# Kernel tuning notes

Hardware: AMD Instinct MI355X
Metric: run time of the kernel (lower is better)

## Reference

```python
import jax, jax.numpy as jnp
import numpy as np

N_PATCHES = 14
N_BLOCKS = 12
HIDDEN = 768
N_HEADS = 12
D_HEAD = HIDDEN // N_HEADS
MLP_RATIO = 4
OUT_D = 1000
BATCH = 32
C, H, W = 3, 224, 224
PS = H // N_PATCHES            # 16
INPUT_D = C * PS * PS          # 768
SEQ = N_PATCHES ** 2 + 1       # 197
LN_EPS = 1e-5


def _pos_emb(length, d):
    i = np.arange(length, dtype=np.float64)[:, None]
    j = np.arange(d, dtype=np.float64)[None, :]
    angle = i / (10000.0 ** ((j - (j % 2)) / d))
    pe = np.where(j % 2 == 0, np.sin(angle), np.cos(angle))
    return jnp.asarray(pe, dtype=jnp.float32)  # [length, d]


def setup_inputs() -> dict:
    key = jax.random.key(0)
    ks = jax.random.split(key, 16)
    s = 0.02
    inp = {
        "x": jax.random.normal(ks[0], (BATCH, C, H, W), jnp.float32),
        "W_map": jax.random.normal(ks[1], (INPUT_D, HIDDEN), jnp.float32) * s,
        "b_map": jnp.zeros((HIDDEN,), jnp.float32),
        "cls_tok": jax.random.uniform(ks[2], (1, HIDDEN), jnp.float32),
        "pos_emb": _pos_emb(SEQ, HIDDEN),
        "ln1_s": jnp.ones((N_BLOCKS, HIDDEN), jnp.float32),
        "ln1_b": jnp.zeros((N_BLOCKS, HIDDEN), jnp.float32),
        "Wq": jax.random.normal(ks[3], (N_BLOCKS, N_HEADS, D_HEAD, D_HEAD), jnp.float32) * s,
        "bq": jnp.zeros((N_BLOCKS, N_HEADS, D_HEAD), jnp.float32),
        "Wk": jax.random.normal(ks[4], (N_BLOCKS, N_HEADS, D_HEAD, D_HEAD), jnp.float32) * s,
        "bk": jnp.zeros((N_BLOCKS, N_HEADS, D_HEAD), jnp.float32),
        "Wv": jax.random.normal(ks[5], (N_BLOCKS, N_HEADS, D_HEAD, D_HEAD), jnp.float32) * s,
        "bv": jnp.zeros((N_BLOCKS, N_HEADS, D_HEAD), jnp.float32),
        "ln2_s": jnp.ones((N_BLOCKS, HIDDEN), jnp.float32),
        "ln2_b": jnp.zeros((N_BLOCKS, HIDDEN), jnp.float32),
        "W1": jax.random.normal(ks[6], (N_BLOCKS, HIDDEN, MLP_RATIO * HIDDEN), jnp.float32) * s,
        "b1": jnp.zeros((N_BLOCKS, MLP_RATIO * HIDDEN), jnp.float32),
        "W2": jax.random.normal(ks[7], (N_BLOCKS, MLP_RATIO * HIDDEN, HIDDEN), jnp.float32) * s,
        "b2": jnp.zeros((N_BLOCKS, HIDDEN), jnp.float32),
        "W_out": jax.random.normal(ks[8], (HIDDEN, OUT_D), jnp.float32) * s,
        "b_out": jnp.zeros((OUT_D,), jnp.float32),
    }
    return inp


def _layernorm(x, scale, bias):
    m = jnp.mean(x, axis=-1, keepdims=True)
    v = jnp.mean(jnp.square(x - m), axis=-1, keepdims=True)
    return (x - m) * jax.lax.rsqrt(v + LN_EPS) * scale + bias


def _patchify(x):
    # [N,C,H,W] -> [N, np*np, C*ps*ps], channel-major flatten per patch (matches torch flatten)
    n = x.shape[0]
    p = x.reshape(n, C, N_PATCHES, PS, N_PATCHES, PS)
    p = p.transpose(0, 2, 4, 1, 3, 5)  # [N, np, np, C, ps, ps]
    return p.reshape(n, N_PATCHES * N_PATCHES, INPUT_D)


def _msa(x, Wq, bq, Wk, bk, Wv, bv):
    # x: [N,S,D]; per-head separate linears, faithful scale = 1/sqrt(n_heads)
    n, s_, _ = x.shape
    xh = x.reshape(n, s_, N_HEADS, D_HEAD)
    q = jnp.einsum('nshd,hde->nhse', xh, Wq) + bq[None, :, None, :]
    k = jnp.einsum('nshd,hde->nhse', xh, Wk) + bk[None, :, None, :]
    v = jnp.einsum('nshd,hde->nhse', xh, Wv) + bv[None, :, None, :]
    scale = 1.0 / jnp.sqrt(jnp.float32(N_HEADS))
    att = jax.nn.softmax(jnp.einsum('nhse,nhte->nhst', q, k) * scale, axis=-1)
    o = jnp.einsum('nhst,nhte->nhse', att, v)
    return o.transpose(0, 2, 1, 3).reshape(n, s_, HIDDEN)


def reference(x, W_map, b_map, cls_tok, pos_emb, ln1_s, ln1_b, Wq, bq, Wk, bk, Wv, bv,
              ln2_s, ln2_b, W1, b1, W2, b2, W_out, b_out):
    n = x.shape[0]
    tokens = _patchify(x) @ W_map + b_map                       # [N, np^2, D]
    tokens = jnp.concatenate([jnp.broadcast_to(cls_tok[None], (n, 1, HIDDEN)), tokens], axis=1)
    h = tokens + pos_emb[None]                                  # [N, S, D]
    for blk in range(N_BLOCKS):
        attn_out = _msa(_layernorm(h, ln1_s[blk], ln1_b[blk]),
                        Wq[blk], bq[blk], Wk[blk], bk[blk], Wv[blk], bv[blk])
        out = h + attn_out
        # faithful to source: MLP branch reads norm2(x), not norm2(out)
        m = _layernorm(h, ln2_s[blk], ln2_b[blk])
        m = jax.nn.gelu(m @ W1[blk] + b1[blk], approximate=False) @ W2[blk] + b2[blk]
        h = out + m
    cls = h[:, 0]                                               # [N, D]
    return jax.nn.softmax(cls @ W_out + b_out, axis=1)          # [N, out_d]
```

## Files before the change

### kernel.cpp

```cpp
#include <hip/hip_runtime.h>
#include <math.h>

#define BATCH   32
#define SEQ     197
#define HIDDEN  768
#define NHEADS  12
#define DHEAD   64
#define NBLOCKS 12
#define MLP_D   3072
#define OUTD    1000
#define NPATCH  196
#define M_TOK   (BATCH*SEQ)
#define M_PAD   6400
#define LN_EPS  1e-5f
#define SP      208

typedef _Float16 f16;
typedef _Float16 f16x8 __attribute__((ext_vector_type(8)));
typedef _Float16 f16x4 __attribute__((ext_vector_type(4)));
typedef float    f32x4 __attribute__((ext_vector_type(4)));

__device__ __forceinline__ float gelu_exact(float x) {
    return 0.5f * x * (1.0f + erff(x * 0.70710678118654752f));
}

__device__ __forceinline__ void gload_lds16(const void* g, void* l) {
    __builtin_amdgcn_global_load_lds(
        (const __attribute__((address_space(1))) void*)g,
        (__attribute__((address_space(3))) void*)l, 16, 0, 0);
}

__device__ __forceinline__ f16x8 lds_ld(const char* base, int row, int rs, int kbyte) {
    return *(const f16x8*)(base + row*rs + (kbyte ^ ((row & 7) << 4)));
}

__device__ __forceinline__ f16x8 lds32(const char* buf, int row, int lg) {
    int p = row >> 1;
    int sl = (((row & 1) << 2) + lg) ^ (p & 7);
    return *(const f16x8*)(buf + p*128 + sl*16);
}

__global__ __launch_bounds__(256) void patchify_kernel(const float* __restrict__ x,
                                                       f16* __restrict__ patches) {
    int row = blockIdx.x;
    int n = row / NPATCH;
    int p = row % NPATCH;
    int pi = p / 14, pj = p % 14;
    for (int k = threadIdx.x; k < 768; k += 256) {
        int c   = k >> 8;
        int r   = (k >> 4) & 15;
        int col = k & 15;
        patches[(size_t)row*768 + k] =
            (f16)x[(((size_t)n*3 + c)*224 + (pi*16 + r))*224 + pj*16 + col];
    }
}

__global__ __launch_bounds__(256) void transT_kernel(const float* __restrict__ src,
                                                     f16* __restrict__ dst,
                                                     int R, int C) {
    const float* in = src + (size_t)blockIdx.z * R * C;
    f16* out = dst + (size_t)blockIdx.z * R * C;
    __shared__ float tile[64][65];
    int r0 = blockIdx.y * 64, c0 = blockIdx.x * 64;
    int t = threadIdx.x;
    int lr16 = t >> 4, lc4 = (t & 15) * 4;
    #pragma unroll
    for (int i = 0; i < 4; ++i) {
        int r = i*16 + lr16;
        float4 v = *(const float4*)&in[(size_t)(r0 + r)*C + c0 + lc4];
        tile[r][lc4] = v.x; tile[r][lc4+1] = v.y; tile[r][lc4+2] = v.z; tile[r][lc4+3] = v.w;
    }
    __syncthreads();
    #pragma unroll
    for (int i = 0; i < 4; ++i) {
        int c = i*16 + lr16;
        int r = lc4;
        f16x4 pv = { (f16)tile[r][c], (f16)tile[r+1][c], (f16)tile[r+2][c], (f16)tile[r+3][c] };
        *(f16x4*)&out[(size_t)(c0 + c)*R + r0 + r] = pv;
    }
}

__global__ __launch_bounds__(256) void convtrans2_kernel(const float* __restrict__ W1,
                                                         const float* __restrict__ W2,
                                                         f16* __restrict__ W1T,
                                                         f16* __restrict__ W2T) {
    int z = blockIdx.z;
    const float* in = z ? W2 : W1;
    f16* out = z ? W2T : W1T;
    int R = z ? MLP_D : HIDDEN;
    int C = z ? HIDDEN : MLP_D;
    int bx = z ? blockIdx.y : blockIdx.x;
    int by = z ? blockIdx.x : blockIdx.y;
    __shared__ float tile[32][33];
    int r0 = by * 32, c0 = bx * 32;
    int tx = threadIdx.x & 31, ty = threadIdx.x >> 5;
    #pragma unroll
    for (int i = 0; i < 4; ++i) {
        int r = ty + i*8;
        tile[r][tx] = in[(size_t)(r0 + r)*C + c0 + tx];
    }
    __syncthreads();
    #pragma unroll
    for (int i = 0; i < 4; ++i) {
        int r = ty + i*8;
        out[(size_t)(c0 + r)*R + r0 + tx] = (f16)tile[tx][r];
    }
}

__global__ __launch_bounds__(256) void qkvtrans_kernel(const float* __restrict__ Wq,
                                                       const float* __restrict__ Wk,
                                                       const float* __restrict__ Wv,
                                                       f16* __restrict__ outT) {
    int b = blockIdx.x;
    int blkL = b / 36, rem = b % 36;
    int hh = rem / 3, mat = rem % 3;
    const float* in = (mat == 0 ? Wq : mat == 1 ? Wk : Wv) + ((size_t)(blkL*12 + hh))*4096;
    f16* out = outT + (size_t)b * 4096;
    __shared__ float tile[64][65];
    int t = threadIdx.x;
    for (int i = t; i < 4096; i += 256) tile[i >> 6][i & 63] = in[i];
    __syncthreads();
    for (int i = t; i < 4096; i += 256) out[i] = (f16)tile[i & 63][i >> 6];
}

__global__ __launch_bounds__(256) void assemble_kernel(const float* __restrict__ tokens,
                                                       const float* __restrict__ cls,
                                                       const float* __restrict__ pos,
                                                       float* __restrict__ h) {
    int r = blockIdx.x;
    int n = r / SEQ, s = r % SEQ;
    for (int c = threadIdx.x; c < 768; c += 256) {
        float v = (s == 0) ? cls[c] : tokens[(size_t)(n*NPATCH + s - 1)*768 + c];
        h[(size_t)r*768 + c] = v + pos[s*768 + c];
    }
}

__global__ __launch_bounds__(256) void layernorm2_kernel(const float* __restrict__ x,
                                                         const float* __restrict__ s1,
                                                         const float* __restrict__ b1,
                                                         const float* __restrict__ s2,
                                                         const float* __restrict__ b2,
                                                         f16* __restrict__ o1,
                                                         f16* __restrict__ o2) {
    int wid = threadIdx.x >> 6, lane = threadIdx.x & 63;
    int r = blockIdx.x * 4 + wid;
    const float4* xr = (const float4*)(x + (size_t)r * 768);
    float4 v[3];
    v[0] = xr[lane]; v[1] = xr[lane + 64]; v[2] = xr[lane + 128];
    float s = v[0].x+v[0].y+v[0].z+v[0].w + v[1].x+v[1].y+v[1].z+v[1].w
            + v[2].x+v[2].y+v[2].z+v[2].w;
    #pragma unroll
    for (int off = 32; off > 0; off >>= 1) s += __shfl_xor(s, off);
    float mean = s * (1.0f/768.0f);
    float q = 0.f;
    #pragma unroll
    for (int j = 0; j < 3; ++j) {
        float a = v[j].x-mean, b = v[j].y-mean, c = v[j].z-mean, d = v[j].w-mean;
        q += a*a + b*b + c*c + d*d;
    }
    #pragma unroll
    for (int off = 32; off > 0; off >>= 1) q += __shfl_xor(q, off);
    float inv = rsqrtf(q * (1.0f/768.0f) + LN_EPS);
    #pragma unroll
    for (int j = 0; j < 3; ++j) {
        int col = (lane + 64*j) * 4;
        float4 sc1 = *(const float4*)(s1 + col);
        float4 bb1 = *(const float4*)(b1 + col);
        float4 sc2 = *(const float4*)(s2 + col);
        float4 bb2 = *(const float4*)(b2 + col);
        float a = (v[j].x-mean)*inv, b = (v[j].y-mean)*inv,
              c = (v[j].z-mean)*inv, d = (v[j].w-mean)*inv;
        f16x4 w1 = { (f16)(a*sc1.x+bb1.x), (f16)(b*sc1.y+bb1.y),
                     (f16)(c*sc1.z+bb1.z), (f16)(d*sc1.w+bb1.w) };
        f16x4 w2 = { (f16)(a*sc2.x+bb2.x), (f16)(b*sc2.y+bb2.y),
                     (f16)(c*sc2.z+bb2.z), (f16)(d*sc2.w+bb2.w) };
        *(f16x4*)(o1 + (size_t)r*768 + col) = w1;
        *(f16x4*)(o2 + (size_t)r*768 + col) = w2;
    }
}

__global__ __launch_bounds__(512) void fused_attn_kernel(
        const f16* __restrict__ lnh, const f16* __restrict__ qkvT,
        const float* __restrict__ bq, const float* __restrict__ bk,
        const float* __restrict__ bv, float* __restrict__ O) {
    int n = blockIdx.x, h = blockIdx.y;
    int t = threadIdx.x, wid = t >> 6, lane = t & 63;
    int lr = lane & 15;
    int lg = lane >> 4;

    __shared__ char lds[153600];
    char* Xs  = lds;
    char* Qs  = lds + 26624;
    char* Ks  = lds + 53248;
    char* VsT = lds + 79872;
    char* Ws  = lds + 112640;
    char* Ps  = (wid < 3) ? (lds + wid*8192)
              : (wid < 6) ? (lds + 112640 + (wid-3)*8192)
                          : (lds + 137216 + (wid-6)*8192);

    const char* xsrc = (const char*)(lnh + (size_t)n*SEQ*768 + h*64);
    for (int c = t; c < SP*8; c += 512) {
        int s = c >> 3, kb = (c & 7) * 16;
        f16x8 v = {};
        if (s < SEQ) v = *(const f16x8*)(xsrc + (size_t)s*1536 + kb);
        *(f16x8*)(Xs + s*128 + (kb ^ ((s & 7) << 4))) = v;
    }
    const char* wsrc = (const char*)(qkvT) + (size_t)h * 3 * 4096 * 2;
    for (int c = t; c < 1536; c += 512) {
        int byte = c * 16, row = byte >> 7, kb = byte & 127;
        f16x8 v = *(const f16x8*)(wsrc + byte);
        *(f16x8*)(Ws + row*128 + (kb ^ ((row & 7) << 4))) = v;
    }
    for (int c = t; c < 384; c += 512) {
        int e = c / 6, sl = c % 6;
        int kb = 416 + sl * 16;
        *(f16x8*)(VsT + e*512 + (kb ^ ((e & 7) << 4))) = (f16x8){};
    }
    __syncthreads();

    for (int idx = wid; idx < 39; idx += 8) {
        int mat = idx / 13, mt = idx % 13;
        const float* bias = (mat == 0) ? bq : (mat == 1) ? bk : bv;
        #pragma unroll
        for (int nt = 0; nt < 4; ++nt) {
            f32x4 acc = {};
            #pragma unroll
            for (int ks = 0; ks < 2; ++ks) {
                f16x8 a = lds_ld(Xs, mt*16 + lr, 128, lg*16 + ks*64);
                f16x8 b = lds_ld(Ws, mat*64 + nt*16 + lr, 128, lg*16 + ks*64);
                acc = __builtin_amdgcn_mfma_f32_16x16x32_f16(a, b, acc, 0, 0, 0);
            }
            float bb = bias[h*64 + nt*16 + lr];
            if (mat < 2) {
                char* dst = (mat == 0) ? Qs : Ks;
                #pragma unroll
                for (int j = 0; j < 4; ++j) {
                    int s = mt*16 + lg*4 + j;
                    int eb = (nt*16 + lr) * 2;
                    *(f16*)(dst + s*128 + (eb ^ ((s & 7) << 4))) = (f16)(acc[j] + bb);
                }
            } else {
                int e = nt*16 + lr;
                int sb = (mt*16 + lg*4) * 2;
                f16x4 pv;
                #pragma unroll
                for (int j = 0; j < 4; ++j) pv[j] = (f16)(acc[j] + bb);
                *(f16x4*)(VsT + e*512 + (sb ^ ((e & 7) << 4))) = pv;
            }
        }
    }
    __syncthreads();

    for (int c = lane; c < 96; c += 64) {
        int r = c / 6, kb = 416 + (c % 6) * 16;
        *(f16x8*)(Ps + r*512 + (kb ^ ((r & 7) << 4))) = (f16x8){};
    }

    const float scale = 0.28867513459481288f;
    for (int mt = wid; mt < 13; mt += 8) {
        f32x4 sacc[13];
        #pragma unroll
        for (int nt = 0; nt < 13; ++nt) sacc[nt] = (f32x4){};
        #pragma unroll
        for (int ks = 0; ks < 2; ++ks) {
            f16x8 a = lds_ld(Qs, mt*16 + lr, 128, lg*16 + ks*64);
            #pragma unroll
            for (int nt = 0; nt < 13; ++nt) {
                f16x8 b = lds_ld(Ks, nt*16 + lr, 128, lg*16 + ks*64);
                sacc[nt] = __builtin_amdgcn_mfma_f32_16x16x32_f16(a, b, sacc[nt], 0, 0, 0);
            }
        }
        float mx0 = -1e30f, mx1 = -1e30f, mx2 = -1e30f, mx3 = -1e30f;
        #pragma unroll
        for (int nt = 0; nt < 13; ++nt) {
            bool valid = (nt*16 + lr) < SEQ;
            #pragma unroll
            for (int j = 0; j < 4; ++j) {
                float v = valid ? sacc[nt][j] * scale : -1e30f;
                sacc[nt][j] = v;
            }
            mx0 = fmaxf(mx0, sacc[nt][0]); mx1 = fmaxf(mx1, sacc[nt][1]);
            mx2 = fmaxf(mx2, sacc[nt][2]); mx3 = fmaxf(mx3, sacc[nt][3]);
        }
        #pragma unroll
        for (int off = 1; off < 16; off <<= 1) {
            mx0 = fmaxf(mx0, __shfl_xor(mx0, off));
            mx1 = fmaxf(mx1, __shfl_xor(mx1, off));
            mx2 = fmaxf(mx2, __shfl_xor(mx2, off));
            mx3 = fmaxf(mx3, __shfl_xor(mx3, off));
        }
        float s0 = 0.f, s1 = 0.f, s2 = 0.f, s3 = 0.f;
        #pragma unroll
        for (int nt = 0; nt < 13; ++nt) {
            float p0 = expf(sacc[nt][0] - mx0); sacc[nt][0] = p0; s0 += p0;
            float p1 = expf(sacc[nt][1] - mx1); sacc[nt][1] = p1; s1 += p1;
            float p2 = expf(sacc[nt][2] - mx2); sacc[nt][2] = p2; s2 += p2;
            float p3 = expf(sacc[nt][3] - mx3); sacc[nt][3] = p3; s3 += p3;
        }
        #pragma unroll
        for (int off = 1; off < 16; off <<= 1) {
            s0 += __shfl_xor(s0, off); s1 += __shfl_xor(s1, off);
            s2 += __shfl_xor(s2, off); s3 += __shfl_xor(s3, off);
        }
        float i0 = 1.0f/s0, i1 = 1.0f/s1, i2 = 1.0f/s2, i3 = 1.0f/s3;
        #pragma unroll
        for (int nt = 0; nt < 13; ++nt) {
            int cb = (nt*16 + lr) * 2;
            { int r = lg*4 + 0; *(f16*)(Ps + r*512 + (cb ^ ((r & 7) << 4))) = (f16)(sacc[nt][0] * i0); }
            { int r = lg*4 + 1; *(f16*)(Ps + r*512 + (cb ^ ((r & 7) << 4))) = (f16)(sacc[nt][1] * i1); }
            { int r = lg*4 + 2; *(f16*)(Ps + r*512 + (cb ^ ((r & 7) << 4))) = (f16)(sacc[nt][2] * i2); }
            { int r = lg*4 + 3; *(f16*)(Ps + r*512 + (cb ^ ((r & 7) << 4))) = (f16)(sacc[nt][3] * i3); }
        }
        f32x4 oacc[4] = {};
        #pragma unroll
        for (int ks = 0; ks < 8; ++ks) {
            f16x8 a = lds_ld(Ps, lr, 512, lg*16 + ks*64);
            #pragma unroll
            for (int nt = 0; nt < 4; ++nt) {
                f16x8 b = lds_ld(VsT, nt*16 + lr, 512, lg*16 + ks*64);
                oacc[nt] = __builtin_amdgcn_mfma_f32_16x16x32_f16(a, b, oacc[nt], 0, 0, 0);
            }
        }
        #pragma unroll
        for (int nt = 0; nt < 4; ++nt) {
            #pragma unroll
            for (int j = 0; j < 4; ++j) {
                int s = mt*16 + lg*4 + j;
                if (s < SEQ)
                    O[((size_t)(n*SEQ + s))*768 + h*64 + nt*16 + lr] = oacc[nt][j];
            }
        }
    }
}

template<int MODE, int TN>
__global__ __launch_bounds__(256) void hgemm_kernel(
        const f16* __restrict__ A,
        const f16* __restrict__ BT,
        const float* __restrict__ bias,
        const float* __restrict__ res1,
        const float* __restrict__ res2,
        void* __restrict__ Cout, int M, int N, int K, int nbx) {
    constexpr int BISS = TN / 64;
    constexpr int WN   = TN / 2;
    constexpr int NFR  = WN / 16;
    __shared__ f16 As[2][128*32];
    __shared__ f16 Bs[2][TN*32];
    int t = threadIdx.x;
    int wid = t >> 6, lane = t & 63;
    int lr = lane & 15, lg = lane >> 4;
    int wr = wid >> 1, wc = wid & 1;

    int nwg = gridDim.x, bid = blockIdx.x;
    int q = nwg >> 3, r = nwg & 7;
    int xcd = bid & 7, idx = bid >> 3;
    int swz = (xcd < r) ? xcd*(q+1) + idx : r*(q+1) + (xcd-r)*q + idx;
    int bn = (swz % nbx) * TN;
    int bm = (swz / nbx) * 128;

    int agrow[2], agk[2], bgrow[BISS], bgk[BISS];
    #pragma unroll
    for (int i = 0; i < 2; ++i) {
        int fb = i*4096 + wid*1024 + lane*16;
        int p = fb >> 7, u = ((fb >> 4) & 7) ^ (p & 7);
        agrow[i] = 2*p + (u >> 2); agk[i] = (u & 3) * 8;
    }
    #pragma unroll
    for (int i = 0; i < BISS; ++i) {
        int fb = i*4096 + wid*1024 + lane*16;
        int p = fb >> 7, u = ((fb >> 4) & 7) ^ (p & 7);
        bgrow[i] = 2*p + (u >> 2); bgk[i] = (u & 3) * 8;
    }

    #define STAGE(P, K0)                                                          \
        do {                                                                      \
            _Pragma("unroll")                                                     \
            for (int i = 0; i < 2; ++i)                                           \
                gload_lds16(A + (size_t)(bm + agrow[i])*K + (K0) + agk[i],        \
                            (char*)&As[P][0] + i*4096 + wid*1024);                \
            _Pragma("unroll")                                                     \
            for (int i = 0; i < BISS; ++i)                                        \
                gload_lds16(BT + (size_t)(bn + bgrow[i])*K + (K0) + bgk[i],       \
                            (char*)&Bs[P][0] + i*4096 + wid*1024);                \
        } while (0)

    f32x4 acc[4][NFR] = {};
    int nk = K >> 5;

    STAGE(0, 0);
    __syncthreads();
    for (int kt = 0; kt < nk; ++kt) {
        int cur = kt & 1;
        if (kt + 1 < nk) STAGE(cur ^ 1, (kt + 1) * 32);
        const char* Ab = (const char*)&As[cur][0];
        const char* Bb = (const char*)&Bs[cur][0];
        f16x8 a[4], b[NFR];
        #pragma unroll
        for (int m = 0; m < 4; ++m)
            a[m] = lds32(Ab, wr*64 + m*16 + lr, lg);
        #pragma unroll
        for (int nn = 0; nn < NFR; ++nn)
            b[nn] = lds32(Bb, wc*WN + nn*16 + lr, lg);
        #pragma unroll
        for (int m = 0; m < 4; ++m)
            #pragma unroll
            for (int nn = 0; nn < NFR; ++nn)
                acc[m][nn] = __builtin_amdgcn_mfma_f32_16x16x32_f16(a[m], b[nn], acc[m][nn], 0, 0, 0);
        __syncthreads();
    }
    #undef STAGE

    int row0 = bm + wr*64 + lg*4;
    int col0 = bn + wc*WN + lr;
    #pragma unroll
    for (int m = 0; m < 4; ++m) {
        #pragma unroll
        for (int nn = 0; nn < NFR; ++nn) {
            int col = col0 + nn*16;
            float bv = bias[col];
            #pragma unroll
            for (int j = 0; j < 4; ++j) {
                int row = row0 + m*16 + j;
                if (row >= M) continue;
                float v = acc[m][nn][j] + bv;
                size_t idx = (size_t)row*N + col;
                if (MODE == 0) {
                    if (res1) v += res1[idx] + res2[idx];
                    ((float*)Cout)[idx] = v;
                } else {
                    ((f16*)Cout)[idx] = (f16)gelu_exact(v);
                }
            }
        }
    }
}

__global__ __launch_bounds__(256) void head_kernel(const float* __restrict__ h,
                                                   const float* __restrict__ W_out,
                                                   const float* __restrict__ b_out,
                                                   float* __restrict__ out) {
    int n = blockIdx.x, t = threadIdx.x;
    __shared__ float xs[HIDDEN];
    __shared__ float red[4];
    const float* hr = h + (size_t)n*SEQ*HIDDEN;
    for (int k = t; k < HIDDEN; k += 256) xs[k] = hr[k];
    __syncthreads();

    bool v3 = t < (OUTD - 768);
    int c3 = v3 ? (t + 768) : t;
    float a0 = 0.f, a1 = 0.f, a2 = 0.f, a3 = 0.f;
    #pragma unroll 8
    for (int k = 0; k < HIDDEN; ++k) {
        float xv = xs[k];
        const float* wr = W_out + (size_t)k*OUTD;
        a0 = fmaf(xv, wr[t],       a0);
        a1 = fmaf(xv, wr[t + 256], a1);
        a2 = fmaf(xv, wr[t + 512], a2);
        a3 = fmaf(xv, wr[c3],      a3);
    }
    a0 += b_out[t]; a1 += b_out[t + 256]; a2 += b_out[t + 512];
    a3 = v3 ? (a3 + b_out[t + 768]) : -1e30f;

    int wid = t >> 6, lane = t & 63;
    float mx = fmaxf(fmaxf(a0, a1), fmaxf(a2, a3));
    #pragma unroll
    for (int off = 32; off > 0; off >>= 1) mx = fmaxf(mx, __shfl_xor(mx, off));
    if (lane == 0) red[wid] = mx;
    __syncthreads();
    mx = fmaxf(fmaxf(red[0], red[1]), fmaxf(red[2], red[3]));
    __syncthreads();

    float p0 = expf(a0 - mx), p1 = expf(a1 - mx), p2 = expf(a2 - mx);
    float p3 = v3 ? expf(a3 - mx) : 0.f;
    float s = p0 + p1 + p2 + p3;
    #pragma unroll
    for (int off = 32; off > 0; off >>= 1) s += __shfl_xor(s, off);
    if (lane == 0) red[wid] = s;
    __syncthreads();
    s = red[0] + red[1] + red[2] + red[3];
    float inv = 1.0f / s;

    float* orow = out + (size_t)n*OUTD;
    orow[t]       = p0 * inv;
    orow[t + 256] = p1 * inv;
    orow[t + 512] = p2 * inv;
    if (v3) orow[t + 768] = p3 * inv;
}

extern "C" void kernel_launch(void* const* d_in, const int* in_sizes, int n_in,
                              void* d_out, int out_size, void* d_ws, size_t ws_size,
                              hipStream_t stream) {
    const float* x     = (const float*)d_in[0];
    const float* W_map = (const float*)d_in[1];
    const float* b_map = (const float*)d_in[2];
    const float* cls_t = (const float*)d_in[3];
    const float* pos   = (const float*)d_in[4];
    const float* ln1_s = (const float*)d_in[5];
    const float* ln1_b = (const float*)d_in[6];
    const float* Wq    = (const float*)d_in[7];
    const float* bq    = (const float*)d_in[8];
    const float* Wk    = (const float*)d_in[9];
    const float* bk    = (const float*)d_in[10];
    const float* Wv    = (const float*)d_in[11];
    const float* bv    = (const float*)d_in[12];
    const float* ln2_s = (const float*)d_in[13];
    const float* ln2_b = (const float*)d_in[14];
    const float* W1    = (const float*)d_in[15];
    const float* b1    = (const float*)d_in[16];
    const float* W2    = (const float*)d_in[17];
    const float* b2    = (const float*)d_in[18];
    const float* W_out = (const float*)d_in[19];
    const float* b_out = (const float*)d_in[20];
    float* out = (float*)d_out;

    const size_t LAYER_W = (size_t)HIDDEN * MLP_D;

    char* w = (char*)d_ws;
    const size_t SZ32 = (size_t)M_TOK * HIDDEN * 4;
    float* h        = (float*)w;  w += SZ32;
    float* attn_out = (float*)w;  w += SZ32;
    f16*   mid_h    = (f16*)w;    w += (size_t)M_PAD * MLP_D * 2;
    f16*   lnh1     = (f16*)w;    w += (size_t)M_PAD * HIDDEN * 2;
    f16*   lnh2     = (f16*)w;    w += (size_t)M_PAD * HIDDEN * 2;
    f16*   WmapT    = (f16*)w;    w += (size_t)768 * 768 * 2;
    f16*   qkvT     = (f16*)w;    w += (size_t)NBLOCKS * NHEADS * 3 * 64 * 64 * 2;
    size_t base_used = (size_t)(w - (char*)d_ws);
    bool big = ws_size >= base_used + 2 * NBLOCKS * LAYER_W * 2;
    f16* W1T = (f16*)w;  w += (big ? NBLOCKS : 1) * LAYER_W * 2;
    f16* W2T = (f16*)w;  w += (big ? NBLOCKS : 1) * LAYER_W * 2;

    f16* patches_h = mid_h;
    patchify_kernel<<<BATCH*NPATCH, 256, 0, stream>>>(x, patches_h);
    {
        dim3 g(12, 12, 1);
        transT_kernel<<<g, 256, 0, stream>>>(W_map, WmapT, 768, 768);
    }
    qkvtrans_kernel<<<NBLOCKS*NHEADS*3, 256, 0, stream>>>(Wq, Wk, Wv, qkvT);
    if (big) {
        dim3 g1(MLP_D/64, HIDDEN/64, NBLOCKS);
        transT_kernel<<<g1, 256, 0, stream>>>(W1, W1T, HIDDEN, MLP_D);
        dim3 g2(HIDDEN/64, MLP_D/64, NBLOCKS);
        transT_kernel<<<g2, 256, 0, stream>>>(W2, W2T, MLP_D, HIDDEN);
    }
    hgemm_kernel<0,64><<<49*12, 256, 0, stream>>>(patches_h, WmapT, b_map,
                                                  nullptr, nullptr,
                                                  (void*)attn_out, BATCH*NPATCH, 768, 768, 12);
    assemble_kernel<<<M_TOK, 256, 0, stream>>>(attn_out, cls_t, pos, h);

    for (int blk = 0; blk < NBLOCKS; ++blk) {
        f16* w1t = big ? (W1T + (size_t)blk * LAYER_W) : W1T;
        f16* w2t = big ? (W2T + (size_t)blk * LAYER_W) : W2T;
        layernorm2_kernel<<<M_TOK/4, 256, 0, stream>>>(h,
            ln1_s + blk*768, ln1_b + blk*768, ln2_s + blk*768, ln2_b + blk*768,
            lnh1, lnh2);
        if (!big) {
            dim3 g(MLP_D/32, HIDDEN/32, 2);
            convtrans2_kernel<<<g, 256, 0, stream>>>(W1 + (size_t)blk*LAYER_W,
                                                     W2 + (size_t)blk*LAYER_W, w1t, w2t);
        }
        {
            dim3 g(BATCH, NHEADS);
            fused_attn_kernel<<<g, 512, 0, stream>>>(lnh1,
                qkvT + (size_t)blk*NHEADS*3*4096,
                bq + (size_t)blk*768, bk + (size_t)blk*768, bv + (size_t)blk*768,
                attn_out);
        }
        hgemm_kernel<1,64><<<50*48, 256, 0, stream>>>(lnh2, w1t, b1 + (size_t)blk*MLP_D,
                                                      nullptr, nullptr,
                                                      (void*)mid_h, M_TOK, MLP_D, 768, 48);
        hgemm_kernel<0,64><<<50*12, 256, 0, stream>>>(mid_h, w2t, b2 + (size_t)blk*HIDDEN,
                                                      h, attn_out,
                                                      (void*)h, M_TOK, HIDDEN, MLP_D, 12);
    }

    head_kernel<<<BATCH, 256, 0, stream>>>(h, W_out, b_out, out);
}
```

Before: 2.344 ms.

## Add 256x128-tile triple-buffered GEMM kernel for MLP up-projection

Adds a new GEMM kernel for the first MLP projection (W1 + GELU). It uses 512 threads, 256x128 output tiles, a K-step of 64, an XOR-swizzled LDS layout and a three-stage async global-to-LDS pipeline, replacing the 128x64 double-buffered generic kernel. Larger tiles are meant to cut global/L2 traffic per FLOP and the deeper pipeline to hide load latency. In exchange it uses about 144KB of LDS and many accumulator registers per thread, so only one workgroup fits per CU and the grid shrinks to 600 workgroups.

```diff
diff --git a/kernel.cpp b/kernel.cpp
--- a/kernel.cpp
+++ b/kernel.cpp
@@ -335,11 +335,9 @@
 
 template<int MODE, int TN>
 __global__ __launch_bounds__(256) void hgemm_kernel(
-        const f16* __restrict__ A,
-        const f16* __restrict__ BT,
+        const f16* __restrict__ A, const f16* __restrict__ BT,
         const float* __restrict__ bias,
-        const float* __restrict__ res1,
-        const float* __restrict__ res2,
+        const float* __restrict__ res1, const float* __restrict__ res2,
         void* __restrict__ Cout, int M, int N, int K, int nbx) {
     constexpr int BISS = TN / 64;
     constexpr int WN   = TN / 2;
@@ -430,6 +428,103 @@
                 } else {
                     ((f16*)Cout)[idx] = (f16)gelu_exact(v);
                 }
+            }
+        }
+    }
+}
+
+__global__ __launch_bounds__(512) void hgemm9_kernel(
+        const f16* __restrict__ A,
+        const f16* __restrict__ BT,
+        const float* __restrict__ bias,
+        f16* __restrict__ Cout,
+        int M, int N, int K, int nbx) {
+    __shared__ f16 As[3][256*64];
+    __shared__ f16 Bs[3][128*64];
+    int t = threadIdx.x;
+    int wid = t >> 6, lane = t & 63;
+    int lr = lane & 15, lg = lane >> 4;
+    int wr = wid >> 2, wc = wid & 3;
+
+    int nwg = gridDim.x, bid = blockIdx.x;
+    int q = nwg >> 3, r = nwg & 7;
+    int xcd = bid & 7, idx = bid >> 3;
+    int swz = (xcd < r) ? xcd*(q+1) + idx : r*(q+1) + (xcd-r)*q + idx;
+    int bn = (swz % nbx) * 128;
+    int bm = (swz / nbx) * 256;
+
+    int arow[4], akk[4], brow[2], bkk[2];
+    #pragma unroll
+    for (int i = 0; i < 4; ++i) {
+        int fb = i*8192 + t*16;
+        int row = fb >> 7, sl = (fb >> 4) & 7;
+        arow[i] = row; akk[i] = (sl ^ (row & 7)) * 8;
+    }
+    #pragma unroll
+    for (int i = 0; i < 2; ++i) {
+        int fb = i*8192 + t*16;
+        int row = fb >> 7, sl = (fb >> 4) & 7;
+        brow[i] = row; bkk[i] = (sl ^ (row & 7)) * 8;
+    }
+
+    #define STAGE9(P, K0)                                                         \
+        do {                                                                      \
+            _Pragma("unroll")                                                     \
+            for (int i = 0; i < 4; ++i)                                           \
+                gload_lds16(A + (size_t)(bm + arow[i])*K + (K0) + akk[i],         \
+                            (char*)&As[P][0] + i*8192 + wid*1024);                \
+            _Pragma("unroll")                                                     \
+            for (int i = 0; i < 2; ++i)                                           \
+                gload_lds16(BT + (size_t)(bn + brow[i])*K + (K0) + bkk[i],        \
+                            (char*)&Bs[P][0] + i*8192 + wid*1024);                \
+        } while (0)
+
+    f32x4 acc[8][2] = {};
+    int nk = K >> 6;
+
+    STAGE9(0, 0);
+    STAGE9(1, 64);
+    for (int kt = 0; kt < nk; ++kt) {
+        int cur = kt % 3;
+        if (kt + 1 < nk) asm volatile("s_waitcnt vmcnt(6)" ::: "memory");
+        else             asm volatile("s_waitcnt vmcnt(0)" ::: "memory");
+        __builtin_amdgcn_s_barrier();
+        asm volatile("" ::: "memory");
+        if (kt + 2 < nk) STAGE9((kt + 2) % 3, (kt + 2) * 64);
+        const char* Ab = (const char*)&As[cur][0];
+        const char* Bb = (const char*)&Bs[cur][0];
+        #pragma unroll
+        for (int kh = 0; kh < 2; ++kh) {
+            f16x8 a[8], b[2];
+            #pragma unroll
+            for (int nn = 0; nn < 2; ++nn)
+                b[nn] = lds_ld(Bb, wc*32 + nn*16 + lr, 128, lg*16 + kh*64);
+            #pragma unroll
+            for (int m = 0; m < 8; ++m)
+                a[m] = lds_ld(Ab, wr*128 + m*16 + lr, 128, lg*16 + kh*64);
+            #pragma unroll
+            for (int m = 0; m < 8; ++m)
+                #pragma unroll
+                for (int nn = 0; nn < 2; ++nn)
+                    acc[m][nn] = __builtin_amdgcn_mfma_f32_16x16x32_f16(a[m], b[nn], acc[m][nn], 0, 0, 0);
+        }
+        asm volatile("" ::: "memory");
+    }
+    #undef STAGE9
+
+    int row0 = bm + wr*128 + lg*4;
+    int col0 = bn + wc*32 + lr;
+    #pragma unroll
+    for (int m = 0; m < 8; ++m) {
+        #pragma unroll
+        for (int nn = 0; nn < 2; ++nn) {
+            int col = col0 + nn*16;
+            float bv = bias[col];
+            #pragma unroll
+            for (int j = 0; j < 4; ++j) {
+                int row = row0 + m*16 + j;
+                if (row >= M) continue;
+                Cout[(size_t)row*N + col] = (f16)gelu_exact(acc[m][nn][j] + bv);
             }
         }
     }
@@ -565,9 +660,8 @@
                 bq + (size_t)blk*768, bk + (size_t)blk*768, bv + (size_t)blk*768,
                 attn_out);
         }
-        hgemm_kernel<1,64><<<50*48, 256, 0, stream>>>(lnh2, w1t, b1 + (size_t)blk*MLP_D,
-                                                      nullptr, nullptr,
-                                                      (void*)mid_h, M_TOK, MLP_D, 768, 48);
+        hgemm9_kernel<<<25*24, 512, 0, stream>>>(lnh2, w1t, b1 + (size_t)blk*MLP_D,
+                                                 mid_h, M_TOK, MLP_D, 768, 24);
         hgemm_kernel<0,64><<<50*12, 256, 0, stream>>>(mid_h, w2t, b2 + (size_t)blk*HIDDEN,
                                                       h, attn_out,
                                                       (void*)h, M_TOK, HIDDEN, MLP_D, 12);
```

Measured after the change: 2.675 ms. 1.14x slower.

## Enlarge GEMM tiles to 256x128 with 512-thread workgroups

Applied to the files above, without the earlier changes.

Replaces the 128xTN GEMM kernel with a 256x128 tile kernel that uses 8 waves (2x4) per workgroup, each wave computing 128x32. The larger tile raises arithmetic intensity and cuts global loads of A and B per output element. The grid shrinks accordingly, to 150 workgroups for the N=768 GEMMs and 600 for the MLP up-projection. The risk is lower occupancy and fewer workgroups than CUs on the N=768 GEMMs, which can leave the device underfilled. The patch-embed GEMM has M=6272, and relies on padded buffers for the tile rows past M.

```diff
diff --git a/kernel.cpp b/kernel.cpp
--- a/kernel.cpp
+++ b/kernel.cpp
@@ -333,43 +333,39 @@
     }
 }
 
-template<int MODE, int TN>
-__global__ __launch_bounds__(256) void hgemm_kernel(
+template<int MODE>
+__global__ __launch_bounds__(512) void hgemm10_kernel(
         const f16* __restrict__ A,
         const f16* __restrict__ BT,
         const float* __restrict__ bias,
         const float* __restrict__ res1,
         const float* __restrict__ res2,
         void* __restrict__ Cout, int M, int N, int K, int nbx) {
-    constexpr int BISS = TN / 64;
-    constexpr int WN   = TN / 2;
-    constexpr int NFR  = WN / 16;
-    __shared__ f16 As[2][128*32];
-    __shared__ f16 Bs[2][TN*32];
+    __shared__ f16 As[2][256*32];
+    __shared__ f16 Bs[2][128*32];
     int t = threadIdx.x;
     int wid = t >> 6, lane = t & 63;
     int lr = lane & 15, lg = lane >> 4;
-    int wr = wid >> 1, wc = wid & 1;
+    int wr = wid >> 2, wc = wid & 3;
 
     int nwg = gridDim.x, bid = blockIdx.x;
     int q = nwg >> 3, r = nwg & 7;
     int xcd = bid & 7, idx = bid >> 3;
     int swz = (xcd < r) ? xcd*(q+1) + idx : r*(q+1) + (xcd-r)*q + idx;
-    int bn = (swz % nbx) * TN;
-    int bm = (swz / nbx) * 128;
-
-    int agrow[2], agk[2], bgrow[BISS], bgk[BISS];
+    int bn = (swz % nbx) * 128;
+    int bm = (swz / nbx) * 256;
+
+    int agrow[2], agk[2], bgrow, bgk;
     #pragma unroll
     for (int i = 0; i < 2; ++i) {
-        int fb = i*4096 + wid*1024 + lane*16;
+        int fb = i*8192 + t*16;
         int p = fb >> 7, u = ((fb >> 4) & 7) ^ (p & 7);
         agrow[i] = 2*p + (u >> 2); agk[i] = (u & 3) * 8;
     }
-    #pragma unroll
-    for (int i = 0; i < BISS; ++i) {
-        int fb = i*4096 + wid*1024 + lane*16;
+    {
+        int fb = t*16;
         int p = fb >> 7, u = ((fb >> 4) & 7) ^ (p & 7);
-        bgrow[i] = 2*p + (u >> 2); bgk[i] = (u & 3) * 8;
+        bgrow = 2*p + (u >> 2); bgk = (u & 3) * 8;
     }
 
     #define STAGE(P, K0)                                                          \
@@ -377,14 +373,12 @@
             _Pragma("unroll")                                                     \
             for (int i = 0; i < 2; ++i)                                           \
                 gload_lds16(A + (size_t)(bm + agrow[i])*K + (K0) + agk[i],        \
-                            (char*)&As[P][0] + i*4096 + wid*1024);                \
-            _Pragma("unroll")                                                     \
-            for (int i = 0; i < BISS; ++i)                                        \
-                gload_lds16(BT + (size_t)(bn + bgrow[i])*K + (K0) + bgk[i],       \
-                            (char*)&Bs[P][0] + i*4096 + wid*1024);                \
+                            (char*)&As[P][0] + i*8192 + wid*1024);                \
+            gload_lds16(BT + (size_t)(bn + bgrow)*K + (K0) + bgk,                 \
+                        (char*)&Bs[P][0] + wid*1024);                             \
         } while (0)
 
-    f32x4 acc[4][NFR] = {};
+    f32x4 acc[8][2] = {};
     int nk = K >> 5;
 
     STAGE(0, 0);
@@ -394,28 +388,28 @@
         if (kt + 1 < nk) STAGE(cur ^ 1, (kt + 1) * 32);
         const char* Ab = (const char*)&As[cur][0];
         const char* Bb = (const char*)&Bs[cur][0];
-        f16x8 a[4], b[NFR];
-        #pragma unroll
-        for (int m = 0; m < 4; ++m)
-            a[m] = lds32(Ab, wr*64 + m*16 + lr, lg);
-        #pragma unroll
-        for (int nn = 0; nn < NFR; ++nn)
-            b[nn] = lds32(Bb, wc*WN + nn*16 + lr, lg);
-        #pragma unroll
-        for (int m = 0; m < 4; ++m)
-            #pragma unroll
-            for (int nn = 0; nn < NFR; ++nn)
+        f16x8 a[8], b[2];
+        #pragma unroll
+        for (int m = 0; m < 8; ++m)
+            a[m] = lds32(Ab, wr*128 + m*16 + lr, lg);
+        #pragma unroll
+        for (int nn = 0; nn < 2; ++nn)
+            b[nn] = lds32(Bb, wc*32 + nn*16 + lr, lg);
+        #pragma unroll
+        for (int m = 0; m < 8; ++m)
+            #pragma unroll
+            for (int nn = 0; nn < 2; ++nn)
                 acc[m][nn] = __builtin_amdgcn_mfma_f32_16x16x32_f16(a[m], b[nn], acc[m][nn], 0, 0, 0);
         __syncthreads();
     }
     #undef STAGE
 
-    int row0 = bm + wr*64 + lg*4;
-    int col0 = bn + wc*WN + lr;
-    #pragma unroll
-    for (int m = 0; m < 4; ++m) {
-        #pragma unroll
-        for (int nn = 0; nn < NFR; ++nn) {
+    int row0 = bm + wr*128 + lg*4;
+    int col0 = bn + wc*32 + lr;
+    #pragma unroll
+    for (int m = 0; m < 8; ++m) {
+        #pragma unroll
+        for (int nn = 0; nn < 2; ++nn) {
             int col = col0 + nn*16;
             float bv = bias[col];
             #pragma unroll
@@ -542,9 +536,9 @@
         dim3 g2(HIDDEN/64, MLP_D/64, NBLOCKS);
         transT_kernel<<<g2, 256, 0, stream>>>(W2, W2T, MLP_D, HIDDEN);
     }
-    hgemm_kernel<0,64><<<49*12, 256, 0, stream>>>(patches_h, WmapT, b_map,
-                                                  nullptr, nullptr,
-                                                  (void*)attn_out, BATCH*NPATCH, 768, 768, 12);
+    hgemm10_kernel<0><<<25*6, 512, 0, stream>>>(patches_h, WmapT, b_map,
+                                                nullptr, nullptr,
+                                                (void*)attn_out, BATCH*NPATCH, 768, 768, 6);
     assemble_kernel<<<M_TOK, 256, 0, stream>>>(attn_out, cls_t, pos, h);
 
     for (int blk = 0; blk < NBLOCKS; ++blk) {
@@ -565,12 +559,12 @@
                 bq + (size_t)blk*768, bk + (size_t)blk*768, bv + (size_t)blk*768,
                 attn_out);
         }
-        hgemm_kernel<1,64><<<50*48, 256, 0, stream>>>(lnh2, w1t, b1 + (size_t)blk*MLP_D,
-                                                      nullptr, nullptr,
-                                                      (void*)mid_h, M_TOK, MLP_D, 768, 48);
-        hgemm_kernel<0,64><<<50*12, 256, 0, stream>>>(mid_h, w2t, b2 + (size_t)blk*HIDDEN,
-                                                      h, attn_out,
-                                                      (void*)h, M_TOK, HIDDEN, MLP_D, 12);
+        hgemm10_kernel<1><<<25*24, 512, 0, stream>>>(lnh2, w1t, b1 + (size_t)blk*MLP_D,
+                                                     nullptr, nullptr,
+                                                     (void*)mid_h, M_TOK, MLP_D, 768, 24);
+        hgemm10_kernel<0><<<25*6, 512, 0, stream>>>(mid_h, w2t, b2 + (size_t)blk*HIDDEN,
+                                                    h, attn_out,
+                                                    (void*)h, M_TOK, HIDDEN, MLP_D, 6);
     }
 
     head_kernel<<<BATCH, 256, 0, stream>>>(h, W_out, b_out, out);
```

After: 2.589 ms. 10.5% more time.
